# Kernel optimization log

Measured on AMD Instinct MI355X. Metric: run time of the kernel, lower is better.

Reference implementation:

```python
import jax, jax.numpy as jnp
import numpy as np

K = 3          # kernel_size
STRIDE = 2
PAD = K // 2


def setup_inputs() -> dict:
    key = jax.random.key(0)
    k1, k2, k3 = jax.random.split(key, 3)
    B, C, H, W = 8, 64, 256, 256
    x = jax.random.normal(k1, (B, C, H, W), dtype=jnp.float32)
    # conv_sigma: Conv2d(C, C//2, 3, bias=False), kaiming_normal-ish scale
    w_sigma = jax.random.normal(k2, (C // 2, C, 3, 3), dtype=jnp.float32) * (2.0 / (9 * C)) ** 0.5
    # fc: Linear(C//2, 1)
    w_fc = jax.random.normal(k3, (1, C // 2), dtype=jnp.float32) * 0.1
    b_fc = jnp.zeros((1,), dtype=jnp.float32)
    return {"x": x, "w_sigma": w_sigma, "w_fc": w_fc, "b_fc": b_fc}


def _gaussian_kernels(sigma):
    # sigma: [B, 1] -> normalized Gaussian kernels [B, 1, K, K]
    r = jnp.arange(-PAD, PAD + 1, dtype=jnp.float32)
    d = jnp.sqrt(r[:, None] ** 2 + r[None, :] ** 2)          # [K, K] radial distance
    s = jnp.clip(sigma, 1e-4)[:, :, None, None]              # [B, 1, 1, 1]
    g = (1.0 / (jnp.sqrt(2.0 * jnp.pi) * s)) * jnp.exp(-0.5 * (d / s) ** 2)
    return g / jnp.sum(g, axis=(2, 3), keepdims=True)


def reference(x, w_sigma, w_fc, b_fc):
    B = x.shape[0]
    # sigma branch: 3x3 VALID conv -> relu -> global avgpool -> fc -> sigmoid
    h = jax.lax.conv_general_dilated(
        x, w_sigma, (1, 1), 'VALID',
        dimension_numbers=('NCHW', 'OIHW', 'NCHW'))           # [B, C/2, H-2, W-2]
    h = jax.nn.relu(h).mean(axis=(2, 3))                      # [B, C/2]
    sigma = jax.nn.sigmoid(h @ w_fc.T + b_fc)                 # [B, 1]
    kern = _gaussian_kernels(sigma)                           # [B, 1, K, K]
    # per-sample blur: treat C as batch, B as channels, grouped conv groups=B
    xp = jnp.pad(x.transpose(1, 0, 2, 3),
                 ((0, 0), (0, 0), (PAD, PAD), (PAD, PAD)), mode='reflect')
    out = jax.lax.conv_general_dilated(
        xp, kern, (STRIDE, STRIDE), 'VALID',
        dimension_numbers=('NCHW', 'OIHW', 'NCHW'),
        feature_group_count=B)                                # [C, B, H', W']
    return out
```

## Files before the change

### kernel.cpp

```cpp
#include <hip/hip_runtime.h>
#include <math.h>


typedef __attribute__((ext_vector_type(8))) short s8v;
typedef __attribute__((ext_vector_type(4))) float f4v;

static __device__ inline unsigned short f2bf(float f) {
    union { float f; unsigned int u; } v; v.f = f;
    unsigned int u = v.u;
    unsigned int r = u + 0x7FFFu + ((u >> 16) & 1u);
    return (unsigned short)(r >> 16);
}

static __device__ inline unsigned int pk_bf16(float a, float b) {
    unsigned int r;
    asm("v_cvt_pk_bf16_f32 %0, %1, %2" : "=v"(r) : "v"(a), "v"(b));
    return r;
}

__global__ void prep_kernel(const float* __restrict__ w, float* __restrict__ ws) {
    int i = blockIdx.x * blockDim.x + threadIdx.x;
    if (i < 256) ws[i] = 0.f;
    if (i < 9 * 32 * 64) {
        int ic  = i & 63;
        int oc  = (i >> 6) & 31;
        int tap = i >> 11;
        unsigned short* wtb = (unsigned short*)(ws + 512);
        wtb[i] = f2bf(w[oc * 576 + ic * 9 + tap]);
    }
}

__global__ __launch_bounds__(256, 3) void conv_mfma_kernel(
        const float* __restrict__ x, const unsigned short* __restrict__ wtb,
        float* __restrict__ acc_out) {
    __shared__ __align__(16) unsigned char sx[370 * 128];
    __shared__ float sred[4][32];

    const int bx = blockIdx.x, by = blockIdx.y, b = blockIdx.z;
    const int ox0 = bx * 32, oy0 = by * 8;
    const int tid = threadIdx.x;
    const int lane = tid & 63, w = tid >> 6;
    const int m = lane & 15, q = lane >> 4;

    const float* xb = x + (size_t)b * 64 * 65536;
    float4 va[6][4];
    int   pj[6];
    int   r4a[6];
    bool  vld[6];
#pragma unroll
    for (int k = 0; k < 6; ++k) {
        int i  = tid + k * 256;
        int ch = i % 9;
        int t9 = i / 9;
        int yy = t9 % 10;
        int r4 = t9 / 10;
        int y  = oy0 + yy;  if (y > 255) y = 255;
        int xc = ox0 + ch * 4;  if (xc > 252) xc = 252;
        const float* src = xb + (size_t)((r4 & 15) << 2) * 65536 + y * 256 + xc;
        va[k][0] = *(const float4*)(src);
        va[k][1] = *(const float4*)(src + 65536);
        va[k][2] = *(const float4*)(src + 131072);
        va[k][3] = *(const float4*)(src + 196608);
        pj[k]  = yy * 37 + ch * 4;
        r4a[k] = r4;
        vld[k] = (i < 1440);
    }

    const unsigned short* wB = wtb + m * 64 + q * 8;
    s8v bc0 = *(const s8v*)(wB);
    s8v bc1 = *(const s8v*)(wB + 1024);
    s8v bc2 = *(const s8v*)(wB + 32);
    s8v bc3 = *(const s8v*)(wB + 1024 + 32);

#pragma unroll
    for (int k = 0; k < 6; ++k) {
        if (vld[k]) {
            int r4 = r4a[k];
            const float* a0 = (const float*)&va[k][0];
            const float* a1 = (const float*)&va[k][1];
            const float* a2 = (const float*)&va[k][2];
            const float* a3 = (const float*)&va[k][3];
#pragma unroll
            for (int j = 0; j < 4; ++j) {
                int p = pj[k] + j;
                unsigned int lo = pk_bf16(a0[j], a1[j]);
                unsigned int hi = pk_bf16(a2[j], a3[j]);
                int cw = (r4 >> 1) ^ ((p >> 1) & 7);
                *(uint2*)(sx + p * 128 + cw * 16 + (r4 & 1) * 8) = make_uint2(lo, hi);
            }
        }
    }
    __syncthreads();

    f4v acc[4][2];
#pragma unroll
    for (int mt = 0; mt < 4; ++mt)
#pragma unroll
        for (int nt = 0; nt < 2; ++nt) acc[mt][nt] = (f4v)0.f;

    int pb[4];
#pragma unroll
    for (int mt = 0; mt < 4; ++mt)
        pb[mt] = (2 * w + (mt >> 1)) * 37 + (mt & 1) * 16 + m;

#pragma unroll
    for (int t = 0; t < 9; ++t) {
        const int off = (t / 3) * 37 + (t % 3);
        s8v bn0, bn1, bn2, bn3;
        if (t < 8) {
            const unsigned short* wN = wB + (t + 1) * 2048;
            bn0 = *(const s8v*)(wN);
            bn1 = *(const s8v*)(wN + 1024);
            bn2 = *(const s8v*)(wN + 32);
            bn3 = *(const s8v*)(wN + 1024 + 32);
        }
#pragma unroll
        for (int mt = 0; mt < 4; ++mt) {
            int p  = pb[mt] + off;
            int q0 = q ^ ((p >> 1) & 7);
            s8v afr = *(const s8v*)(sx + p * 128 + q0 * 16);
            acc[mt][0] = __builtin_amdgcn_mfma_f32_16x16x32_bf16(afr, bc0, acc[mt][0], 0, 0, 0);
            acc[mt][1] = __builtin_amdgcn_mfma_f32_16x16x32_bf16(afr, bc1, acc[mt][1], 0, 0, 0);
        }
#pragma unroll
        for (int mt = 0; mt < 4; ++mt) {
            int p  = pb[mt] + off;
            int q1 = (4 + q) ^ ((p >> 1) & 7);
            s8v afr = *(const s8v*)(sx + p * 128 + q1 * 16);
            acc[mt][0] = __builtin_amdgcn_mfma_f32_16x16x32_bf16(afr, bc2, acc[mt][0], 0, 0, 0);
            acc[mt][1] = __builtin_amdgcn_mfma_f32_16x16x32_bf16(afr, bc3, acc[mt][1], 0, 0, 0);
        }
        if (t < 8) { bc0 = bn0; bc1 = bn1; bc2 = bn2; bc3 = bn3; }
    }

    float s0 = 0.f, s1 = 0.f;
#pragma unroll
    for (int mt = 0; mt < 4; ++mt) {
        int oy = oy0 + 2 * w + (mt >> 1);
        int oxb = ox0 + (mt & 1) * 16 + q * 4;
#pragma unroll
        for (int reg = 0; reg < 4; ++reg) {
            bool val = (oxb + reg < 254) && (oy < 254);
            if (val) {
                s0 += fmaxf(acc[mt][0][reg], 0.f);
                s1 += fmaxf(acc[mt][1][reg], 0.f);
            }
        }
    }
    s0 += __shfl_xor(s0, 16, 64); s0 += __shfl_xor(s0, 32, 64);
    s1 += __shfl_xor(s1, 16, 64); s1 += __shfl_xor(s1, 32, 64);
    if (lane < 16) { sred[w][lane] = s0; sred[w][16 + lane] = s1; }
    __syncthreads();
    if (tid < 32)
        atomicAdd(&acc_out[b * 32 + tid],
                  sred[0][tid] + sred[1][tid] + sred[2][tid] + sred[3][tid]);
}

__global__ void sigma_kernel(const float* __restrict__ acc, const float* __restrict__ wfc,
                             const float* __restrict__ bfc, float* __restrict__ kout) {
    int t = threadIdx.x;
    int b = t >> 3, j = t & 7;
    float s = 0.f;
#pragma unroll
    for (int i = 0; i < 4; ++i) s += acc[b * 32 + j + i * 8] * wfc[j + i * 8];
    s += __shfl_xor(s, 4, 8);
    s += __shfl_xor(s, 2, 8);
    s += __shfl_xor(s, 1, 8);
    if (j == 0) {
        float z = s * (1.0f / (254.0f * 254.0f)) + bfc[0];
        float sig = 1.0f / (1.0f + __expf(-z));
        float ss = fmaxf(sig, 1e-4f);
        float inv2 = 0.5f / (ss * ss);
        float e1 = __expf(-inv2);
        float e2 = __expf(-2.0f * inv2);
        float inv_norm = 1.0f / (1.0f + 4.0f * e1 + 4.0f * e2);
        kout[b * 4 + 0] = inv_norm;
        kout[b * 4 + 1] = e1 * inv_norm;
        kout[b * 4 + 2] = e2 * inv_norm;
    }
}

__global__ __launch_bounds__(256) void blur_kernel(
        const float* __restrict__ x, const float* __restrict__ kp,
        float* __restrict__ out) {
    const int c = blockIdx.z, b = blockIdx.y;
    const int tid = threadIdx.x;
    const int qx = tid & 31;
    const int oy = blockIdx.x * 8 + (tid >> 5);

    const float kC = kp[b * 4 + 0];
    const float kE = kp[b * 4 + 1];
    const float kD = kp[b * 4 + 2];

    const float* xb = x + ((size_t)(b * 64 + c)) * 65536;

    float o0 = 0.f, o1 = 0.f, o2 = 0.f, o3 = 0.f;
#pragma unroll
    for (int dy = 0; dy < 3; ++dy) {
        int iy = 2 * oy + dy - 1;
        if (iy < 0) iy = 1;
        const float* row = xb + iy * 256;
        const float4 f0 = *(const float4*)(row + 8 * qx);
        const float4 f1 = *(const float4*)(row + 8 * qx + 4);
        float lf = __shfl_up(f1.w, 1, 64);
        const float sm1 = (qx == 0) ? f0.y : lf;
        const float ka = (dy == 1) ? kE : kD;
        const float kb = (dy == 1) ? kC : kE;
        const float kc2 = (dy == 1) ? kE : kD;
        o0 = fmaf(ka, sm1,  fmaf(kb, f0.x, fmaf(kc2, f0.y, o0)));
        o1 = fmaf(ka, f0.y, fmaf(kb, f0.z, fmaf(kc2, f0.w, o1)));
        o2 = fmaf(ka, f0.w, fmaf(kb, f1.x, fmaf(kc2, f1.y, o2)));
        o3 = fmaf(ka, f1.y, fmaf(kb, f1.z, fmaf(kc2, f1.w, o3)));
    }
    *(float4*)(out + (((size_t)c * 8 + b) * 128 + oy) * 128 + 4 * qx) =
        make_float4(o0, o1, o2, o3);
}

extern "C" void kernel_launch(void* const* d_in, const int* in_sizes, int n_in,
                              void* d_out, int out_size, void* d_ws, size_t ws_size,
                              hipStream_t stream) {
    const float* x       = (const float*)d_in[0];
    const float* w_sigma = (const float*)d_in[1];
    const float* w_fc    = (const float*)d_in[2];
    const float* b_fc    = (const float*)d_in[3];
    float* out = (float*)d_out;
    float* ws  = (float*)d_ws;
    const unsigned short* wtb = (const unsigned short*)(ws + 512);

    prep_kernel<<<72, 256, 0, stream>>>(w_sigma, ws);
    conv_mfma_kernel<<<dim3(8, 32, 8), 256, 0, stream>>>(x, wtb, ws);
    sigma_kernel<<<1, 64, 0, stream>>>(ws, w_fc, b_fc, ws + 256);
    blur_kernel<<<dim3(16, 8, 64), 256, 0, stream>>>(x, ws + 256, out);
}
```

Baseline: 255.6 us.

## Pre-convert input to NHWC bf16 and stage conv tiles via direct global-to-LDS loads

Result: slower. 288.6 us (+12.9%).

```diff
diff --git a/kernel.cpp b/kernel.cpp
--- a/kernel.cpp
+++ b/kernel.cpp
@@ -17,6 +17,167 @@
     asm("v_cvt_pk_bf16_f32 %0, %1, %2" : "=v"(r) : "v"(a), "v"(b));
     return r;
 }
+
+
+__global__ __launch_bounds__(256) void prep_cvt_kernel(
+        const float* __restrict__ x, const float* __restrict__ w,
+        float* __restrict__ ws, unsigned short* __restrict__ xbf) {
+    const int blk = blockIdx.x;
+    const int tid = threadIdx.x;
+    if (blk >= 8192) {
+        if (tid < 256) ws[tid] = 0.f;
+        unsigned short* wtb = (unsigned short*)(ws + 512);
+        for (int i = tid; i < 9 * 32 * 64; i += 256) {
+            int ic  = i & 63;
+            int oc  = (i >> 6) & 31;
+            int tap = i >> 11;
+            wtb[i] = f2bf(w[oc * 576 + ic * 9 + tap]);
+        }
+        return;
+    }
+    __shared__ __align__(16) unsigned short sld[4096];
+    const int b  = blk >> 10;
+    const int P0 = (blk & 1023) * 64;
+    const float* xb = x + (size_t)b * 64 * 65536;
+
+    const int c = tid & 15, r = tid >> 4;
+#pragma unroll
+    for (int kk = 0; kk < 4; ++kk) {
+        int ic = kk * 16 + r;
+        float4 v = *(const float4*)(xb + (size_t)ic * 65536 + P0 + 4 * c);
+        unsigned int u0 = pk_bf16(v.x, v.y);
+        unsigned int u1 = pk_bf16(v.z, v.w);
+        int slot = c ^ r;
+        *(uint2*)((unsigned char*)sld + ic * 128 + slot * 8) = make_uint2(u0, u1);
+    }
+    __syncthreads();
+
+    const int l = tid & 63, wv = tid >> 6;
+    const int oct = l & 7;
+#pragma unroll
+    for (int k2 = 0; k2 < 2; ++k2) {
+        int px = wv * 16 + k2 * 8 + (l >> 3);
+        unsigned int lo0, lo1, hi0, hi1;
+        unsigned short us[8];
+#pragma unroll
+        for (int i = 0; i < 8; ++i) {
+            int ic = oct * 8 + i;
+            int slot = (px >> 2) ^ (ic & 15);
+            us[i] = *(const unsigned short*)((unsigned char*)sld + ic * 128 + slot * 8 + (px & 3) * 2);
+        }
+        uint4 o4;
+        o4.x = (unsigned int)us[0] | ((unsigned int)us[1] << 16);
+        o4.y = (unsigned int)us[2] | ((unsigned int)us[3] << 16);
+        o4.z = (unsigned int)us[4] | ((unsigned int)us[5] << 16);
+        o4.w = (unsigned int)us[6] | ((unsigned int)us[7] << 16);
+        *(uint4*)(xbf + (((size_t)b * 65536 + P0 + px) * 64 + oct * 8)) = o4;
+    }
+}
+
+__global__ __launch_bounds__(256, 3) void conv_lds_kernel(
+        const unsigned short* __restrict__ xbf,
+        const unsigned short* __restrict__ wtb,
+        float* __restrict__ acc_out) {
+    __shared__ __align__(16) unsigned char sx[360 * 128];
+    __shared__ float sred[4][32];
+
+    const int bx = blockIdx.x, by = blockIdx.y, b = blockIdx.z;
+    const int ox0 = bx * 32, oy0 = by * 8;
+    const int tid = threadIdx.x;
+    const int lane = tid & 63, w = tid >> 6;
+    const int m = lane & 15, q = lane >> 4;
+
+    const unsigned short* wB = wtb + m * 64 + q * 8;
+    s8v bc0 = *(const s8v*)(wB);
+    s8v bc1 = *(const s8v*)(wB + 1024);
+    s8v bc2 = *(const s8v*)(wB + 32);
+    s8v bc3 = *(const s8v*)(wB + 1024 + 32);
+
+    const unsigned short* xb = xbf + (size_t)b * (65536 * 64);
+#pragma unroll
+    for (int cg0 = 0; cg0 < 48; cg0 += 4) {
+        int cg = cg0 + w;
+        if (cg < 45) {
+            int g = cg * 64 + lane;
+            int p = g >> 3, s = g & 7;
+            int yy = p / 36;
+            int xx = p - yy * 36;
+            int y  = oy0 + yy;  if (y  > 255) y  = 255;
+            int xc = ox0 + xx;  if (xc > 255) xc = 255;
+            int o  = s ^ ((p >> 1) & 7);
+            const unsigned short* src = xb + (((y << 8) + xc) << 6) + (o << 3);
+            __builtin_amdgcn_global_load_lds(
+                (const __attribute__((address_space(1))) void*)src,
+                (__attribute__((address_space(3))) void*)(sx + cg * 1024),
+                16, 0, 0);
+        }
+    }
+    __syncthreads();
+
+    f4v acc[4][2];
+#pragma unroll
+    for (int mt = 0; mt < 4; ++mt)
+#pragma unroll
+        for (int nt = 0; nt < 2; ++nt) acc[mt][nt] = (f4v)0.f;
+
+    int pb[4];
+#pragma unroll
+    for (int mt = 0; mt < 4; ++mt)
+        pb[mt] = (2 * w + (mt >> 1)) * 36 + (mt & 1) * 16 + m;
+
+#pragma unroll
+    for (int t = 0; t < 9; ++t) {
+        const int off = (t / 3) * 36 + (t % 3);
+        s8v bn0, bn1, bn2, bn3;
+        if (t < 8) {
+            const unsigned short* wN = wB + (t + 1) * 2048;
+            bn0 = *(const s8v*)(wN);
+            bn1 = *(const s8v*)(wN + 1024);
+            bn2 = *(const s8v*)(wN + 32);
+            bn3 = *(const s8v*)(wN + 1024 + 32);
+        }
+#pragma unroll
+        for (int mt = 0; mt < 4; ++mt) {
+            int p  = pb[mt] + off;
+            int q0 = q ^ ((p >> 1) & 7);
+            s8v afr = *(const s8v*)(sx + p * 128 + q0 * 16);
+            acc[mt][0] = __builtin_amdgcn_mfma_f32_16x16x32_bf16(afr, bc0, acc[mt][0], 0, 0, 0);
+            acc[mt][1] = __builtin_amdgcn_mfma_f32_16x16x32_bf16(afr, bc1, acc[mt][1], 0, 0, 0);
+        }
+#pragma unroll
+        for (int mt = 0; mt < 4; ++mt) {
+            int p  = pb[mt] + off;
+            int q1 = (4 + q) ^ ((p >> 1) & 7);
+            s8v afr = *(const s8v*)(sx + p * 128 + q1 * 16);
+            acc[mt][0] = __builtin_amdgcn_mfma_f32_16x16x32_bf16(afr, bc2, acc[mt][0], 0, 0, 0);
+            acc[mt][1] = __builtin_amdgcn_mfma_f32_16x16x32_bf16(afr, bc3, acc[mt][1], 0, 0, 0);
+        }
+        if (t < 8) { bc0 = bn0; bc1 = bn1; bc2 = bn2; bc3 = bn3; }
+    }
+
+    float s0 = 0.f, s1 = 0.f;
+#pragma unroll
+    for (int mt = 0; mt < 4; ++mt) {
+        int oy = oy0 + 2 * w + (mt >> 1);
+        int oxb = ox0 + (mt & 1) * 16 + q * 4;
+#pragma unroll
+        for (int reg = 0; reg < 4; ++reg) {
+            bool val = (oxb + reg < 254) && (oy < 254);
+            if (val) {
+                s0 += fmaxf(acc[mt][0][reg], 0.f);
+                s1 += fmaxf(acc[mt][1][reg], 0.f);
+            }
+        }
+    }
+    s0 += __shfl_xor(s0, 16, 64); s0 += __shfl_xor(s0, 32, 64);
+    s1 += __shfl_xor(s1, 16, 64); s1 += __shfl_xor(s1, 32, 64);
+    if (lane < 16) { sred[w][lane] = s0; sred[w][16 + lane] = s1; }
+    __syncthreads();
+    if (tid < 32)
+        atomicAdd(&acc_out[b * 32 + tid],
+                  sred[0][tid] + sred[1][tid] + sred[2][tid] + sred[3][tid]);
+}
+
 
 __global__ void prep_kernel(const float* __restrict__ w, float* __restrict__ ws) {
     int i = blockIdx.x * blockDim.x + threadIdx.x;
@@ -156,6 +317,7 @@
                   sred[0][tid] + sred[1][tid] + sred[2][tid] + sred[3][tid]);
 }
 
+
 __global__ void sigma_kernel(const float* __restrict__ acc, const float* __restrict__ wfc,
                              const float* __restrict__ bfc, float* __restrict__ kout) {
     int t = threadIdx.x;
@@ -227,8 +389,15 @@
     float* ws  = (float*)d_ws;
     const unsigned short* wtb = (const unsigned short*)(ws + 512);
 
-    prep_kernel<<<72, 256, 0, stream>>>(w_sigma, ws);
-    conv_mfma_kernel<<<dim3(8, 32, 8), 256, 0, stream>>>(x, wtb, ws);
+    const size_t need = 16384u * 4u + (size_t)8 * 65536 * 64 * 2;
+    if (ws_size >= need) {
+        unsigned short* xbf = (unsigned short*)(ws + 16384);
+        prep_cvt_kernel<<<8193, 256, 0, stream>>>(x, w_sigma, ws, xbf);
+        conv_lds_kernel<<<dim3(8, 32, 8), 256, 0, stream>>>(xbf, wtb, ws);
+    } else {
+        prep_kernel<<<72, 256, 0, stream>>>(w_sigma, ws);
+        conv_mfma_kernel<<<dim3(8, 32, 8), 256, 0, stream>>>(x, wtb, ws);
+    }
     sigma_kernel<<<1, 64, 0, stream>>>(ws, w_fc, b_fc, ws + 256);
     blur_kernel<<<dim3(16, 8, 64), 256, 0, stream>>>(x, ws + 256, out);
 }
```

## Make conv blocks persistent over four row tiles with register-prefetched next tile

Applied to the files above, without the earlier changes.

New measurement: 323.0 us. 26.4% more time.

```diff
diff --git a/kernel.cpp b/kernel.cpp
--- a/kernel.cpp
+++ b/kernel.cpp
@@ -30,40 +30,33 @@
     }
 }
 
-__global__ __launch_bounds__(256, 3) void conv_mfma_kernel(
+__global__ __launch_bounds__(256, 2) void conv_mfma_kernel(
         const float* __restrict__ x, const unsigned short* __restrict__ wtb,
         float* __restrict__ acc_out) {
     __shared__ __align__(16) unsigned char sx[370 * 128];
     __shared__ float sred[4][32];
 
-    const int bx = blockIdx.x, by = blockIdx.y, b = blockIdx.z;
-    const int ox0 = bx * 32, oy0 = by * 8;
+    const int bx = blockIdx.x, byg = blockIdx.y, b = blockIdx.z;
+    const int ox0 = bx * 32;
     const int tid = threadIdx.x;
     const int lane = tid & 63, w = tid >> 6;
     const int m = lane & 15, q = lane >> 4;
-
     const float* xb = x + (size_t)b * 64 * 65536;
-    float4 va[6][4];
-    int   pj[6];
-    int   r4a[6];
-    bool  vld[6];
+
+    int xc_[6], yy_[6], p0_[6];
+    int r4_[6];
+    bool vld_[6];
 #pragma unroll
     for (int k = 0; k < 6; ++k) {
         int i  = tid + k * 256;
         int ch = i % 9;
         int t9 = i / 9;
-        int yy = t9 % 10;
-        int r4 = t9 / 10;
-        int y  = oy0 + yy;  if (y > 255) y = 255;
+        yy_[k] = t9 % 10;
+        r4_[k] = (t9 / 10) & 15;
         int xc = ox0 + ch * 4;  if (xc > 252) xc = 252;
-        const float* src = xb + (size_t)((r4 & 15) << 2) * 65536 + y * 256 + xc;
-        va[k][0] = *(const float4*)(src);
-        va[k][1] = *(const float4*)(src + 65536);
-        va[k][2] = *(const float4*)(src + 131072);
-        va[k][3] = *(const float4*)(src + 196608);
-        pj[k]  = yy * 37 + ch * 4;
-        r4a[k] = r4;
-        vld[k] = (i < 1440);
+        xc_[k] = xc;
+        p0_[k] = yy_[k] * 37 + ch * 4;
+        vld_[k] = (i < 1440);
     }
 
     const unsigned short* wB = wtb + m * 64 + q * 8;
@@ -72,81 +65,139 @@
     s8v bc2 = *(const s8v*)(wB + 32);
     s8v bc3 = *(const s8v*)(wB + 1024 + 32);
 
-#pragma unroll
-    for (int k = 0; k < 6; ++k) {
-        if (vld[k]) {
-            int r4 = r4a[k];
-            const float* a0 = (const float*)&va[k][0];
-            const float* a1 = (const float*)&va[k][1];
-            const float* a2 = (const float*)&va[k][2];
-            const float* a3 = (const float*)&va[k][3];
-#pragma unroll
-            for (int j = 0; j < 4; ++j) {
-                int p = pj[k] + j;
-                unsigned int lo = pk_bf16(a0[j], a1[j]);
-                unsigned int hi = pk_bf16(a2[j], a3[j]);
-                int cw = (r4 >> 1) ^ ((p >> 1) & 7);
-                *(uint2*)(sx + p * 128 + cw * 16 + (r4 & 1) * 8) = make_uint2(lo, hi);
+    float4 va[6][4];
+
+    {
+        const int oy0 = byg * 32;
+#pragma unroll
+        for (int k = 0; k < 6; ++k) {
+            int y = oy0 + yy_[k];  if (y > 255) y = 255;
+            const float* src = xb + ((size_t)r4_[k] << 2) * 65536 + y * 256 + xc_[k];
+            va[k][0] = *(const float4*)(src);
+            va[k][1] = *(const float4*)(src + 65536);
+            va[k][2] = *(const float4*)(src + 131072);
+            va[k][3] = *(const float4*)(src + 196608);
+        }
+#pragma unroll
+        for (int k = 0; k < 6; ++k) {
+            if (vld_[k]) {
+                int r4 = r4_[k];
+                const float* a0 = (const float*)&va[k][0];
+                const float* a1 = (const float*)&va[k][1];
+                const float* a2 = (const float*)&va[k][2];
+                const float* a3 = (const float*)&va[k][3];
+#pragma unroll
+                for (int j = 0; j < 4; ++j) {
+                    int p = p0_[k] + j;
+                    unsigned int lo = pk_bf16(a0[j], a1[j]);
+                    unsigned int hi = pk_bf16(a2[j], a3[j]);
+                    int cw = (r4 >> 1) ^ ((p >> 1) & 7);
+                    *(uint2*)(sx + p * 128 + cw * 16 + (r4 & 1) * 8) = make_uint2(lo, hi);
+                }
             }
         }
     }
     __syncthreads();
-
-    f4v acc[4][2];
-#pragma unroll
-    for (int mt = 0; mt < 4; ++mt)
-#pragma unroll
-        for (int nt = 0; nt < 2; ++nt) acc[mt][nt] = (f4v)0.f;
 
     int pb[4];
 #pragma unroll
     for (int mt = 0; mt < 4; ++mt)
         pb[mt] = (2 * w + (mt >> 1)) * 37 + (mt & 1) * 16 + m;
 
-#pragma unroll
-    for (int t = 0; t < 9; ++t) {
-        const int off = (t / 3) * 37 + (t % 3);
-        s8v bn0, bn1, bn2, bn3;
-        if (t < 8) {
-            const unsigned short* wN = wB + (t + 1) * 2048;
-            bn0 = *(const s8v*)(wN);
-            bn1 = *(const s8v*)(wN + 1024);
-            bn2 = *(const s8v*)(wN + 32);
-            bn3 = *(const s8v*)(wN + 1024 + 32);
-        }
+    float s0 = 0.f, s1 = 0.f;
+
+#pragma unroll 1
+    for (int t = 0; t < 4; ++t) {
+        const int oy0 = byg * 32 + t * 8;
+
+        if (t < 3) {
+            const int oyN = oy0 + 8;
+#pragma unroll
+            for (int k = 0; k < 6; ++k) {
+                int y = oyN + yy_[k];  if (y > 255) y = 255;
+                const float* src = xb + ((size_t)r4_[k] << 2) * 65536 + y * 256 + xc_[k];
+                va[k][0] = *(const float4*)(src);
+                va[k][1] = *(const float4*)(src + 65536);
+                va[k][2] = *(const float4*)(src + 131072);
+                va[k][3] = *(const float4*)(src + 196608);
+            }
+#pragma unroll
+            for (int k = 0; k < 6; ++k)
+                asm volatile("" :: "v"(va[k][0].x), "v"(va[k][1].x),
+                                   "v"(va[k][2].x), "v"(va[k][3].x));
+        }
+
+        f4v acc[4][2];
+#pragma unroll
+        for (int mt = 0; mt < 4; ++mt)
+#pragma unroll
+            for (int nt = 0; nt < 2; ++nt) acc[mt][nt] = (f4v)0.f;
+
+#pragma unroll
+        for (int tp = 0; tp < 9; ++tp) {
+            const int off = (tp / 3) * 37 + (tp % 3);
+            const unsigned short* wN = wB + ((tp + 1) % 9) * 2048;
+            s8v bn0 = *(const s8v*)(wN);
+            s8v bn1 = *(const s8v*)(wN + 1024);
+            s8v bn2 = *(const s8v*)(wN + 32);
+            s8v bn3 = *(const s8v*)(wN + 1024 + 32);
+#pragma unroll
+            for (int mt = 0; mt < 4; ++mt) {
+                int p  = pb[mt] + off;
+                int q0 = q ^ ((p >> 1) & 7);
+                s8v afr = *(const s8v*)(sx + p * 128 + q0 * 16);
+                acc[mt][0] = __builtin_amdgcn_mfma_f32_16x16x32_bf16(afr, bc0, acc[mt][0], 0, 0, 0);
+                acc[mt][1] = __builtin_amdgcn_mfma_f32_16x16x32_bf16(afr, bc1, acc[mt][1], 0, 0, 0);
+            }
+#pragma unroll
+            for (int mt = 0; mt < 4; ++mt) {
+                int p  = pb[mt] + off;
+                int q1 = (4 + q) ^ ((p >> 1) & 7);
+                s8v afr = *(const s8v*)(sx + p * 128 + q1 * 16);
+                acc[mt][0] = __builtin_amdgcn_mfma_f32_16x16x32_bf16(afr, bc2, acc[mt][0], 0, 0, 0);
+                acc[mt][1] = __builtin_amdgcn_mfma_f32_16x16x32_bf16(afr, bc3, acc[mt][1], 0, 0, 0);
+            }
+            bc0 = bn0; bc1 = bn1; bc2 = bn2; bc3 = bn3;
+        }
+
 #pragma unroll
         for (int mt = 0; mt < 4; ++mt) {
-            int p  = pb[mt] + off;
-            int q0 = q ^ ((p >> 1) & 7);
-            s8v afr = *(const s8v*)(sx + p * 128 + q0 * 16);
-            acc[mt][0] = __builtin_amdgcn_mfma_f32_16x16x32_bf16(afr, bc0, acc[mt][0], 0, 0, 0);
-            acc[mt][1] = __builtin_amdgcn_mfma_f32_16x16x32_bf16(afr, bc1, acc[mt][1], 0, 0, 0);
-        }
-#pragma unroll
-        for (int mt = 0; mt < 4; ++mt) {
-            int p  = pb[mt] + off;
-            int q1 = (4 + q) ^ ((p >> 1) & 7);
-            s8v afr = *(const s8v*)(sx + p * 128 + q1 * 16);
-            acc[mt][0] = __builtin_amdgcn_mfma_f32_16x16x32_bf16(afr, bc2, acc[mt][0], 0, 0, 0);
-            acc[mt][1] = __builtin_amdgcn_mfma_f32_16x16x32_bf16(afr, bc3, acc[mt][1], 0, 0, 0);
-        }
-        if (t < 8) { bc0 = bn0; bc1 = bn1; bc2 = bn2; bc3 = bn3; }
-    }
-
-    float s0 = 0.f, s1 = 0.f;
-#pragma unroll
-    for (int mt = 0; mt < 4; ++mt) {
-        int oy = oy0 + 2 * w + (mt >> 1);
-        int oxb = ox0 + (mt & 1) * 16 + q * 4;
-#pragma unroll
-        for (int reg = 0; reg < 4; ++reg) {
-            bool val = (oxb + reg < 254) && (oy < 254);
-            if (val) {
-                s0 += fmaxf(acc[mt][0][reg], 0.f);
-                s1 += fmaxf(acc[mt][1][reg], 0.f);
-            }
-        }
-    }
+            int oy = oy0 + 2 * w + (mt >> 1);
+            int oxb = ox0 + (mt & 1) * 16 + q * 4;
+#pragma unroll
+            for (int reg = 0; reg < 4; ++reg) {
+                bool val = (oxb + reg < 254) && (oy < 254);
+                if (val) {
+                    s0 += fmaxf(acc[mt][0][reg], 0.f);
+                    s1 += fmaxf(acc[mt][1][reg], 0.f);
+                }
+            }
+        }
+
+        if (t < 3) {
+            __syncthreads();
+#pragma unroll
+            for (int k = 0; k < 6; ++k) {
+                if (vld_[k]) {
+                    int r4 = r4_[k];
+                    const float* a0 = (const float*)&va[k][0];
+                    const float* a1 = (const float*)&va[k][1];
+                    const float* a2 = (const float*)&va[k][2];
+                    const float* a3 = (const float*)&va[k][3];
+#pragma unroll
+                    for (int j = 0; j < 4; ++j) {
+                        int p = p0_[k] + j;
+                        unsigned int lo = pk_bf16(a0[j], a1[j]);
+                        unsigned int hi = pk_bf16(a2[j], a3[j]);
+                        int cw = (r4 >> 1) ^ ((p >> 1) & 7);
+                        *(uint2*)(sx + p * 128 + cw * 16 + (r4 & 1) * 8) = make_uint2(lo, hi);
+                    }
+                }
+            }
+            __syncthreads();
+        }
+    }
+
     s0 += __shfl_xor(s0, 16, 64); s0 += __shfl_xor(s0, 32, 64);
     s1 += __shfl_xor(s1, 16, 64); s1 += __shfl_xor(s1, 32, 64);
     if (lane < 16) { sred[w][lane] = s0; sred[w][16 + lane] = s1; }
@@ -228,7 +279,7 @@
     const unsigned short* wtb = (const unsigned short*)(ws + 512);
 
     prep_kernel<<<72, 256, 0, stream>>>(w_sigma, ws);
-    conv_mfma_kernel<<<dim3(8, 32, 8), 256, 0, stream>>>(x, wtb, ws);
+    conv_mfma_kernel<<<dim3(8, 8, 8), 256, 0, stream>>>(x, wtb, ws);
     sigma_kernel<<<1, 64, 0, stream>>>(ws, w_fc, b_fc, ws + 256);
     blur_kernel<<<dim3(16, 8, 64), 256, 0, stream>>>(x, ws + 256, out);
 }
```
